# Kernel optimization log

Hardware: AMD Instinct MI355X
Metric: run time of the kernel (lower is better)

The kernel has to match this reference:

```python
import jax, jax.numpy as jnp
import numpy as np

INP_DIM = 1024
PROJ_DIM = 1024
SEQ = 2048
BATCH = 4

def setup_inputs() -> dict:
    key = jax.random.key(0)
    k1, k2, k3, k4 = jax.random.split(key, 4)
    inputs = jax.random.normal(k1, (BATCH, SEQ, INP_DIM), dtype=jnp.float32)
    # nn.Linear weights stored as (out, in); we keep them that way and transpose in matmul
    Wq = jax.random.normal(k2, (PROJ_DIM, INP_DIM), dtype=jnp.float32) * (1.0 / np.sqrt(INP_DIM))
    Wk = jax.random.normal(k3, (PROJ_DIM, INP_DIM), dtype=jnp.float32) * (1.0 / np.sqrt(INP_DIM))
    Wv = jax.random.normal(k4, (PROJ_DIM, INP_DIM), dtype=jnp.float32) * (1.0 / np.sqrt(INP_DIM))
    return {"inputs": inputs, "Wq": Wq, "Wk": Wk, "Wv": Wv}

def reference(inputs, Wq, Wk, Wv):
    # QKV projections: x @ W.T (nn.Linear convention)
    Q = jnp.einsum('bsd,pd->bsp', inputs, Wq)
    K = jnp.einsum('bsd,pd->bsp', inputs, Wk)
    V = jnp.einsum('bsd,pd->bsp', inputs, Wv)
    scores = jnp.einsum('bqp,bkp->bqk', Q, K)  # [B, S, S]
    n = inputs.shape[1]
    causal = jnp.tril(jnp.ones((n, n), dtype=bool))  # True = keep
    scores = jnp.where(causal, scores, -jnp.inf)
    weights = jax.nn.softmax(scores / jnp.sqrt(jnp.float32(Q.shape[-1])), axis=-1)
    # dropout rate = 0.0 -> identity
    Z = jnp.einsum('bqk,bkp->bqp', weights, V)
    return Z
```

## Files before the change

kernel.cpp:

```cpp
#include <hip/hip_runtime.h>
#include <stdint.h>

#define SEQ   2048
#define DIM   1024
#define BATCH 4

typedef _Float16 f16;
typedef __attribute__((ext_vector_type(8))) _Float16 f16x8;
typedef __attribute__((ext_vector_type(4))) _Float16 f16x4;
typedef __attribute__((ext_vector_type(4))) float   f32x4;

typedef void __attribute__((address_space(1))) vg_t;
typedef void __attribute__((address_space(3))) vl_t;

__device__ __forceinline__ void gld16(const void* g, void* l) {
  __builtin_amdgcn_global_load_lds((vg_t*)g, (vl_t*)l, 16, 0, 0);
}

__global__ __launch_bounds__(256) void cvt_all(const float* __restrict__ x,
                                               const float* __restrict__ wq,
                                               const float* __restrict__ wk,
                                               const float* __restrict__ wv,
                                               f16* __restrict__ xb,
                                               f16* __restrict__ wh) {
  const int bx = blockIdx.x;
  const float* in; f16* out; int base;
  if (bx < 8192)       { in = x;  out = xb;             base = bx; }
  else if (bx < 9216)  { in = wq; out = wh;             base = bx - 8192; }
  else if (bx < 10240) { in = wk; out = wh + (1 << 20); base = bx - 9216; }
  else                 { in = wv; out = wh + (2 << 20); base = bx - 10240; }
  const long i = ((long)base * 256 + threadIdx.x) * 4;
  float4 v = *(const float4*)(in + i);
  f16x4 o = { (f16)v.x, (f16)v.y, (f16)v.z, (f16)v.w };
  *(f16x4*)(out + i) = o;
}

template <int MODE, int CAUSAL, int BK>
__global__ __launch_bounds__(256) void gemm_bt(const f16* __restrict__ A, int lda, long aOffZ,
                                               const f16* __restrict__ B, int ldb, long bOffZ,
                                               void* __restrict__ Cv, int ldc, long cOffZ,
                                               int K) {
  constexpr int CH  = BK / 8;
  constexpr int RPL = 64 / CH;
  constexpr int NL  = 32 / RPL;
  __shared__ __align__(16) f16 lA[128 * BK];
  __shared__ __align__(16) f16 lB[128 * BK];

  const int tid  = threadIdx.x;
  const int wave = tid >> 6;
  const int lane = tid & 63;

  int m0, n0, z;
  if (CAUSAL == 3) {
    const int id   = blockIdx.x;
    const int item = (id < 256) ? id : 767 - id;
    const int mt   = 15 - (item >> 5);
    const int j    = item & 31;
    m0 = mt * 128;
    n0 = (j & 7) * 128;
    z  = j >> 3;
  } else {
    m0 = blockIdx.x * 128;
    n0 = blockIdx.y * 128;
    z  = blockIdx.z;
  }

  if (CAUSAL == 1 && n0 >= m0 + 128) return;
  const int Keff = (CAUSAL >= 2) ? (m0 + 128) : K;

  const f16* Ab = A + (long)z * aOffZ + (long)m0 * lda;
  const f16* Bb = B + (long)z * bOffZ + (long)n0 * ldb;

  const int wm = (wave & 1) * 64;
  const int wn = (wave >> 1) * 64;

  f32x4 acc[4][4] = {};

  const int srow = lane / CH;
  const int sj   = lane % CH;
  const int fr   = lane & 15;
  const int fq   = lane >> 4;

  for (int kt = 0; kt < Keff; kt += BK) {
    __syncthreads();
#pragma unroll
    for (int j = 0; j < NL; ++j) {
      const int rgrp = j * 4 + wave;
      const int row  = rgrp * RPL + srow;
      const int gch  = sj ^ (row & (CH - 1));
      gld16(Ab + (long)row * lda + kt + gch * 8, (void*)(lA + rgrp * 512 + lane * 8));
      gld16(Bb + (long)row * ldb + kt + gch * 8, (void*)(lB + rgrp * 512 + lane * 8));
    }
    __syncthreads();

#pragma unroll
    for (int kk = 0; kk < BK; kk += 32) {
      f16x8 af[4], bf[4];
#pragma unroll
      for (int i = 0; i < 4; ++i) {
        const int arow = wm + i * 16 + fr;
        const int ach  = (kk / 8 + fq) ^ (arow & (CH - 1));
        af[i] = *(const f16x8*)(lA + arow * BK + ach * 8);
        const int brow = wn + i * 16 + fr;
        const int bch  = (kk / 8 + fq) ^ (brow & (CH - 1));
        bf[i] = *(const f16x8*)(lB + brow * BK + bch * 8);
      }
#pragma unroll
      for (int mi = 0; mi < 4; ++mi)
#pragma unroll
        for (int ni = 0; ni < 4; ++ni)
          acc[mi][ni] = __builtin_amdgcn_mfma_f32_16x16x32_f16(af[mi], bf[ni], acc[mi][ni], 0, 0, 0);
    }
  }

#pragma unroll
  for (int mi = 0; mi < 4; ++mi) {
    const int row = m0 + wm + mi * 16 + fq * 4;
#pragma unroll
    for (int ni = 0; ni < 4; ++ni) {
      const int col = n0 + wn + ni * 16 + fr;
      if constexpr (MODE == 0) {
        float* C = (float*)Cv + (long)z * cOffZ;
#pragma unroll
        for (int r = 0; r < 4; ++r) C[(long)(row + r) * ldc + col] = acc[mi][ni][r];
      } else if constexpr (MODE == 1) {
        f16* C = (f16*)Cv + (long)z * cOffZ;
#pragma unroll
        for (int r = 0; r < 4; ++r) C[(long)(row + r) * ldc + col] = (f16)acc[mi][ni][r];
      } else if constexpr (MODE == 2) {
        f16* C = (f16*)Cv + (long)z * cOffZ;
        f16x4 o = { (f16)acc[mi][ni][0], (f16)acc[mi][ni][1],
                    (f16)acc[mi][ni][2], (f16)acc[mi][ni][3] };
        *(f16x4*)(C + (long)col * ldc + row) = o;
      } else {
        f16* Qh  = (f16*)Cv;
        f16* Kh  = Qh + (size_t)8 * 1024 * 1024;
        f16* VTb = Kh + (size_t)8 * 1024 * 1024;
        if (col < 1024) {
#pragma unroll
          for (int r = 0; r < 4; ++r) Qh[(long)(row + r) * DIM + col] = (f16)acc[mi][ni][r];
        } else if (col < 2048) {
#pragma unroll
          for (int r = 0; r < 4; ++r) Kh[(long)(row + r) * DIM + (col - 1024)] = (f16)acc[mi][ni][r];
        } else {
          f16x4 o = { (f16)acc[mi][ni][0], (f16)acc[mi][ni][1],
                      (f16)acc[mi][ni][2], (f16)acc[mi][ni][3] };
          *(f16x4*)(VTb + (long)(col - 2048) * (BATCH * SEQ) + row) = o;
        }
      }
    }
  }
}

__global__ __launch_bounds__(256) void softmax_causal(f16* S) {
  const int q = blockIdx.x, b = blockIdx.y;
  f16* row = S + ((long)b * SEQ + q) * SEQ;
  const int tid = threadIdx.x;
  const int lane = tid & 63, wave = tid >> 6;
  const int nvalid = q + 1;

  f16x8 vv = {};
  if (tid * 8 < nvalid) vv = *(const f16x8*)(row + tid * 8);
  float v[8];
  float m = -3.0e38f;
#pragma unroll
  for (int i = 0; i < 8; ++i) {
    const int k = tid * 8 + i;
    v[i] = (k < nvalid) ? (float)vv[i] * 0.03125f : -3.0e38f;
    m = fmaxf(m, v[i]);
  }
#pragma unroll
  for (int off = 32; off; off >>= 1) m = fmaxf(m, __shfl_xor(m, off));
  __shared__ float redm[4], reds[4];
  if (lane == 0) redm[wave] = m;
  __syncthreads();
  m = fmaxf(fmaxf(redm[0], redm[1]), fmaxf(redm[2], redm[3]));

  float s = 0.f;
#pragma unroll
  for (int i = 0; i < 8; ++i) {
    const float p = (v[i] > -1.0e37f) ? __expf(v[i] - m) : 0.f;
    v[i] = p;
    s += p;
  }
#pragma unroll
  for (int off = 32; off; off >>= 1) s += __shfl_xor(s, off);
  if (lane == 0) reds[wave] = s;
  __syncthreads();
  s = reds[0] + reds[1] + reds[2] + reds[3];
  const float inv = 1.f / s;
  f16x8 o;
#pragma unroll
  for (int i = 0; i < 8; ++i) o[i] = (f16)(v[i] * inv);
  *(f16x8*)(row + tid * 8) = o;
}

extern "C" void kernel_launch(void* const* d_in, const int* in_sizes, int n_in,
                              void* d_out, int out_size, void* d_ws, size_t ws_size,
                              hipStream_t stream) {
  const float* x  = (const float*)d_in[0];
  const float* Wq = (const float*)d_in[1];
  const float* Wk = (const float*)d_in[2];
  const float* Wv = (const float*)d_in[3];
  float* out = (float*)d_out;

  if (ws_size < (size_t)51 * 1024 * 1024 * 2) return;

  f16* xb = (f16*)d_ws;
  f16* Wh = xb + (size_t)8 * 1024 * 1024;
  f16* Qh = Wh + (size_t)3 * 1024 * 1024;
  f16* Kh = Qh + (size_t)8 * 1024 * 1024;
  f16* VT = Kh + (size_t)8 * 1024 * 1024;
  f16* Sc = VT + (size_t)8 * 1024 * 1024;

  const long QOFF = (long)SEQ * DIM;
  const long SOFF = (long)SEQ * SEQ;

  cvt_all<<<11264, 256, 0, stream>>>(x, Wq, Wk, Wv, xb, Wh);

  gemm_bt<3, 0, 64><<<dim3(64, 24, 1), 256, 0, stream>>>(xb, DIM, 0, Wh, DIM, 0, Qh, 0, 0, DIM);

  gemm_bt<1, 1, 64><<<dim3(16, 16, 4), 256, 0, stream>>>(Qh, DIM, QOFF, Kh, DIM, QOFF,
                                                         Sc, SEQ, SOFF, DIM);

  softmax_causal<<<dim3(SEQ, BATCH), 256, 0, stream>>>(Sc);

  gemm_bt<0, 3, 64><<<dim3(512, 1, 1), 256, 0, stream>>>(Sc, SEQ, SOFF,
                                                         VT, BATCH * SEQ, SEQ,
                                                         out, DIM, (long)SEQ * DIM, SEQ);
}
```

Before: 255.1 us.

## Add 256x256 eight-wave pipelined QKV GEMM and widen BK for attention GEMMs

```diff
diff --git a/kernel.cpp b/kernel.cpp
--- a/kernel.cpp
+++ b/kernel.cpp
@@ -35,6 +35,145 @@
   *(f16x4*)(out + i) = o;
 }
 
+__global__ __launch_bounds__(512, 2) void qkv_8ph(const f16* __restrict__ A,
+                                                  const f16* __restrict__ B,
+                                                  f16* __restrict__ Qh) {
+  __shared__ __align__(16) f16 ls[4][16384];
+
+  const int tid  = threadIdx.x;
+  const int wave = tid >> 6;
+  const int lane = tid & 63;
+  const int fr   = lane & 15;
+  const int fq   = lane >> 4;
+
+  const int lin = blockIdx.x;
+  const int swz = (lin & 7) * 48 + (lin >> 3);
+  const int m0  = (swz / 12) * 256;
+  const int n0  = (swz % 12) * 256;
+
+  const f16* Ab = A + (long)m0 * DIM;
+  const f16* Bb = B + (long)n0 * DIM;
+
+  const int wm = (wave & 1) * 128;
+  const int wn = (wave >> 1) * 64;
+
+  f16* lA0 = &ls[0][0]; f16* lB0 = &ls[1][0];
+  f16* lA1 = &ls[2][0]; f16* lB1 = &ls[3][0];
+
+  f32x4 acc[8][4] = {};
+  f16x8 af[4][2], b0[2][2], b1[2][2];
+
+#define STAGE(gb, lb, t, h)                                                    \
+  {                                                                            \
+    const int rr_ = tid >> 3, sj_ = tid & 7;                                   \
+    _Pragma("unroll") for (int i_ = 0; i_ < 2; ++i_) {                         \
+      const int row_ = (h) * 128 + i_ * 64 + rr_;                              \
+      gld16(gb + (long)row_ * DIM + (t) * 64 + ((sj_ ^ (row_ & 7)) << 3),      \
+            (void*)((lb) + (h) * 8192 + i_ * 4096 + tid * 8));                 \
+    }                                                                          \
+  }
+
+#define LDA(lsrc, q)                                                           \
+  {                                                                            \
+    _Pragma("unroll") for (int mi_ = 0; mi_ < 4; ++mi_) {                      \
+      const int row_ = wm + (q) * 64 + mi_ * 16 + fr;                          \
+      _Pragma("unroll") for (int x_ = 0; x_ < 2; ++x_)                         \
+        af[mi_][x_] = *(const f16x8*)((lsrc) + row_ * 64 +                     \
+                                      (((x_ * 4 + fq) ^ (row_ & 7)) << 3));    \
+    }                                                                          \
+  }
+
+#define LDB(lsrc, breg, s)                                                     \
+  {                                                                            \
+    _Pragma("unroll") for (int nj_ = 0; nj_ < 2; ++nj_) {                      \
+      const int row_ = wn + (s) * 32 + nj_ * 16 + fr;                          \
+      _Pragma("unroll") for (int x_ = 0; x_ < 2; ++x_)                         \
+        breg[nj_][x_] = *(const f16x8*)((lsrc) + row_ * 64 +                   \
+                                        (((x_ * 4 + fq) ^ (row_ & 7)) << 3));  \
+    }                                                                          \
+  }
+
+#define MM(q, s, breg)                                                         \
+  {                                                                            \
+    __builtin_amdgcn_s_setprio(1);                                             \
+    _Pragma("unroll") for (int mi_ = 0; mi_ < 4; ++mi_)                        \
+    _Pragma("unroll") for (int nj_ = 0; nj_ < 2; ++nj_)                        \
+    _Pragma("unroll") for (int x_ = 0; x_ < 2; ++x_)                           \
+      acc[(q) * 4 + mi_][(s) * 2 + nj_] = __builtin_amdgcn_mfma_f32_16x16x32_f16( \
+          af[mi_][x_], breg[nj_][x_], acc[(q) * 4 + mi_][(s) * 2 + nj_], 0, 0, 0); \
+    __builtin_amdgcn_s_setprio(0);                                             \
+  }
+
+#define BAR() __builtin_amdgcn_s_barrier()
+#define VMW(n) asm volatile("s_waitcnt vmcnt(" #n ")" ::: "memory")
+
+  STAGE(Bb, lB0, 0, 0); STAGE(Ab, lA0, 0, 0);
+  STAGE(Bb, lB0, 0, 1); STAGE(Ab, lA0, 0, 1);
+  STAGE(Bb, lB1, 1, 0); STAGE(Bb, lB1, 1, 1);
+  VMW(4);
+  BAR();
+
+  for (int j = 0; j < 8; ++j) {
+    const int t0 = 2 * j;
+    const bool nl = (j < 7);
+
+    LDA(lA0, 0); LDB(lB0, b0, 0);
+    STAGE(Ab, lA1, t0 + 1, 0);
+    BAR(); MM(0, 0, b0); BAR();
+    LDB(lB0, b1, 1);
+    STAGE(Ab, lA1, t0 + 1, 1);
+    BAR(); MM(0, 1, b1); BAR();
+    LDA(lA0, 1);
+    if (nl) STAGE(Bb, lB0, t0 + 2, 0);
+    BAR(); MM(1, 1, b1); BAR();
+    if (nl) STAGE(Ab, lA0, t0 + 2, 0);
+    BAR(); MM(1, 0, b0);
+    if (nl) { VMW(4); } else { VMW(0); }
+    BAR();
+    LDA(lA1, 0); LDB(lB1, b0, 0);
+    if (nl) STAGE(Bb, lB0, t0 + 2, 1);
+    BAR(); MM(0, 0, b0); BAR();
+    LDB(lB1, b1, 1);
+    if (nl) STAGE(Ab, lA0, t0 + 2, 1);
+    BAR(); MM(0, 1, b1); BAR();
+    LDA(lA1, 1);
+    if (nl) STAGE(Bb, lB1, t0 + 3, 0);
+    BAR(); MM(1, 1, b1); BAR();
+    if (nl) STAGE(Bb, lB1, t0 + 3, 1);
+    BAR(); MM(1, 0, b0);
+    if (nl) { VMW(4); BAR(); }
+  }
+
+#undef STAGE
+#undef LDA
+#undef LDB
+#undef MM
+#undef BAR
+#undef VMW
+
+  f16* Kh = Qh + (size_t)8 * 1024 * 1024;
+  f16* VT = Kh + (size_t)8 * 1024 * 1024;
+#pragma unroll
+  for (int mi = 0; mi < 8; ++mi) {
+    const int row = m0 + wm + mi * 16 + fq * 4;
+#pragma unroll
+    for (int ni = 0; ni < 4; ++ni) {
+      const int col = n0 + wn + ni * 16 + fr;
+      if (n0 < 1024) {
+#pragma unroll
+        for (int r = 0; r < 4; ++r) Qh[(long)(row + r) * DIM + col] = (f16)acc[mi][ni][r];
+      } else if (n0 < 2048) {
+#pragma unroll
+        for (int r = 0; r < 4; ++r) Kh[(long)(row + r) * DIM + (col - 1024)] = (f16)acc[mi][ni][r];
+      } else {
+        f16x4 o = { (f16)acc[mi][ni][0], (f16)acc[mi][ni][1],
+                    (f16)acc[mi][ni][2], (f16)acc[mi][ni][3] };
+        *(f16x4*)(VT + (long)(col - 2048) * (BATCH * SEQ) + row) = o;
+      }
+    }
+  }
+}
+
 template <int MODE, int CAUSAL, int BK>
 __global__ __launch_bounds__(256) void gemm_bt(const f16* __restrict__ A, int lda, long aOffZ,
                                                const f16* __restrict__ B, int ldb, long bOffZ,
@@ -127,26 +266,11 @@
         f16* C = (f16*)Cv + (long)z * cOffZ;
 #pragma unroll
         for (int r = 0; r < 4; ++r) C[(long)(row + r) * ldc + col] = (f16)acc[mi][ni][r];
-      } else if constexpr (MODE == 2) {
+      } else {
         f16* C = (f16*)Cv + (long)z * cOffZ;
         f16x4 o = { (f16)acc[mi][ni][0], (f16)acc[mi][ni][1],
                     (f16)acc[mi][ni][2], (f16)acc[mi][ni][3] };
         *(f16x4*)(C + (long)col * ldc + row) = o;
-      } else {
-        f16* Qh  = (f16*)Cv;
-        f16* Kh  = Qh + (size_t)8 * 1024 * 1024;
-        f16* VTb = Kh + (size_t)8 * 1024 * 1024;
-        if (col < 1024) {
-#pragma unroll
-          for (int r = 0; r < 4; ++r) Qh[(long)(row + r) * DIM + col] = (f16)acc[mi][ni][r];
-        } else if (col < 2048) {
-#pragma unroll
-          for (int r = 0; r < 4; ++r) Kh[(long)(row + r) * DIM + (col - 1024)] = (f16)acc[mi][ni][r];
-        } else {
-          f16x4 o = { (f16)acc[mi][ni][0], (f16)acc[mi][ni][1],
-                      (f16)acc[mi][ni][2], (f16)acc[mi][ni][3] };
-          *(f16x4*)(VTb + (long)(col - 2048) * (BATCH * SEQ) + row) = o;
-        }
       }
     }
   }
@@ -218,14 +342,14 @@
 
   cvt_all<<<11264, 256, 0, stream>>>(x, Wq, Wk, Wv, xb, Wh);
 
-  gemm_bt<3, 0, 64><<<dim3(64, 24, 1), 256, 0, stream>>>(xb, DIM, 0, Wh, DIM, 0, Qh, 0, 0, DIM);
-
-  gemm_bt<1, 1, 64><<<dim3(16, 16, 4), 256, 0, stream>>>(Qh, DIM, QOFF, Kh, DIM, QOFF,
-                                                         Sc, SEQ, SOFF, DIM);
+  qkv_8ph<<<384, 512, 0, stream>>>(xb, Wh, Qh);
+
+  gemm_bt<1, 1, 128><<<dim3(16, 16, 4), 256, 0, stream>>>(Qh, DIM, QOFF, Kh, DIM, QOFF,
+                                                          Sc, SEQ, SOFF, DIM);
 
   softmax_causal<<<dim3(SEQ, BATCH), 256, 0, stream>>>(Sc);
 
-  gemm_bt<0, 3, 64><<<dim3(512, 1, 1), 256, 0, stream>>>(Sc, SEQ, SOFF,
-                                                         VT, BATCH * SEQ, SEQ,
-                                                         out, DIM, (long)SEQ * DIM, SEQ);
-}
+  gemm_bt<0, 3, 128><<<dim3(512, 1, 1), 256, 0, stream>>>(Sc, SEQ, SOFF,
+                                                          VT, BATCH * SEQ, SEQ,
+                                                          out, DIM, (long)SEQ * DIM, SEQ);
+}
```

New measurement: 237.4 us. 7.0% less time.

## Add triple-buffered 128x256 QKV projection kernel and raise BK for attention GEMMs

Applied to the files above, without the earlier changes.

```diff
diff --git a/kernel.cpp b/kernel.cpp
--- a/kernel.cpp
+++ b/kernel.cpp
@@ -35,6 +35,125 @@
   *(f16x4*)(out + i) = o;
 }
 
+__global__ __launch_bounds__(512, 2) void qkv_p3(const f16* __restrict__ A,
+                                                 const f16* __restrict__ B,
+                                                 f16* __restrict__ Qh) {
+  __shared__ __align__(16) f16 ls[3][24576];
+
+  const int tid  = threadIdx.x;
+  const int wave = tid >> 6;
+  const int lane = tid & 63;
+  const int fr   = lane & 15;
+  const int fq   = lane >> 4;
+
+  const int lin = blockIdx.x;
+  const int swz = (lin & 7) * 96 + (lin >> 3);
+  const int m0  = (swz / 12) * 128;
+  const int n0  = (swz % 12) * 256;
+
+  const f16* Ab = A + (long)m0 * DIM;
+  const f16* Bb = B + (long)n0 * DIM;
+
+  const int wm = (wave & 1) * 64;
+  const int wn = (wave >> 1) * 64;
+
+  f32x4 acc[4][4] = {};
+  f16x8 af[4], bf[4];
+
+#define STAGE(t, c)                                                            \
+  {                                                                            \
+    const int rr_ = tid >> 3, sj_ = tid & 7;                                   \
+    f16* lb_ = &ls[(t) % 3][0];                                                \
+    if ((c) < 2) {                                                             \
+      const int row_ = (c) * 64 + rr_;                                         \
+      gld16(Ab + (long)row_ * DIM + (t) * 64 + ((sj_ ^ (row_ & 7)) << 3),      \
+            (void*)(lb_ + (c) * 4096 + tid * 8));                              \
+    } else {                                                                   \
+      const int row_ = ((c) - 2) * 64 + rr_;                                   \
+      gld16(Bb + (long)row_ * DIM + (t) * 64 + ((sj_ ^ (row_ & 7)) << 3),      \
+            (void*)(lb_ + 8192 + ((c) - 2) * 4096 + tid * 8));                 \
+    }                                                                          \
+  }
+
+#define LDF(p, ks)                                                             \
+  {                                                                            \
+    const f16* lAx_ = &ls[p][0];                                               \
+    const f16* lBx_ = &ls[p][8192];                                            \
+    _Pragma("unroll") for (int mi_ = 0; mi_ < 4; ++mi_) {                      \
+      const int r_ = wm + mi_ * 16 + fr;                                       \
+      af[mi_] = *(const f16x8*)(lAx_ + r_ * 64 +                               \
+                                ((((ks) * 4 + fq) ^ (r_ & 7)) << 3));          \
+    }                                                                          \
+    _Pragma("unroll") for (int ni_ = 0; ni_ < 4; ++ni_) {                      \
+      const int r_ = wn + ni_ * 16 + fr;                                       \
+      bf[ni_] = *(const f16x8*)(lBx_ + r_ * 64 +                               \
+                                ((((ks) * 4 + fq) ^ (r_ & 7)) << 3));          \
+    }                                                                          \
+  }
+
+#define MMAC()                                                                 \
+  {                                                                            \
+    __builtin_amdgcn_s_setprio(1);                                             \
+    _Pragma("unroll") for (int mi_ = 0; mi_ < 4; ++mi_)                        \
+    _Pragma("unroll") for (int ni_ = 0; ni_ < 4; ++ni_)                        \
+      acc[mi_][ni_] = __builtin_amdgcn_mfma_f32_16x16x32_f16(                  \
+          af[mi_], bf[ni_], acc[mi_][ni_], 0, 0, 0);                           \
+    __builtin_amdgcn_s_setprio(0);                                             \
+  }
+
+#define BAR() __builtin_amdgcn_s_barrier()
+#define VMW(n) asm volatile("s_waitcnt vmcnt(" #n ")" ::: "memory")
+
+#pragma unroll
+  for (int c = 0; c < 6; ++c) STAGE(0, c);
+#pragma unroll
+  for (int c = 0; c < 6; ++c) STAGE(1, c);
+  VMW(6);
+  BAR();
+
+#pragma unroll
+  for (int t = 0; t < 14; ++t) {
+    LDF(t % 3, 0);
+    STAGE(t + 2, 0); STAGE(t + 2, 1); STAGE(t + 2, 2);
+    BAR(); MMAC(); BAR();
+    LDF(t % 3, 1);
+    STAGE(t + 2, 3); STAGE(t + 2, 4); STAGE(t + 2, 5);
+    BAR(); MMAC(); VMW(6); BAR();
+  }
+  LDF(2, 0); BAR(); MMAC(); BAR();
+  LDF(2, 1); BAR(); MMAC(); VMW(0); BAR();
+  LDF(0, 0); BAR(); MMAC(); BAR();
+  LDF(0, 1); BAR(); MMAC();
+
+#undef STAGE
+#undef LDF
+#undef MMAC
+#undef BAR
+#undef VMW
+
+  f16* Kh = Qh + (size_t)8 * 1024 * 1024;
+  f16* VT = Kh + (size_t)8 * 1024 * 1024;
+#pragma unroll
+  for (int mi = 0; mi < 4; ++mi) {
+    const int row = m0 + wm + mi * 16 + fq * 4;
+#pragma unroll
+    for (int ni = 0; ni < 4; ++ni) {
+      const int col = n0 + wn + ni * 16 + fr;
+      if (n0 < 1024) {
+#pragma unroll
+        for (int r = 0; r < 4; ++r) Qh[(long)(row + r) * DIM + col] = (f16)acc[mi][ni][r];
+      } else if (n0 < 2048) {
+#pragma unroll
+        for (int r = 0; r < 4; ++r) Kh[(long)(row + r) * DIM + (col - 1024)] = (f16)acc[mi][ni][r];
+      } else {
+        f16x4 o = { (f16)acc[mi][ni][0], (f16)acc[mi][ni][1],
+                    (f16)acc[mi][ni][2], (f16)acc[mi][ni][3] };
+        *(f16x4*)(VT + (long)(col - 2048) * (BATCH * SEQ) + row) = o;
+      }
+    }
+  }
+}
+
 template <int MODE, int CAUSAL, int BK>
 __global__ __launch_bounds__(256) void gemm_bt(const f16* __restrict__ A, int lda, long aOffZ,
                                                const f16* __restrict__ B, int ldb, long bOffZ,
@@ -127,26 +246,11 @@
         f16* C = (f16*)Cv + (long)z * cOffZ;
 #pragma unroll
         for (int r = 0; r < 4; ++r) C[(long)(row + r) * ldc + col] = (f16)acc[mi][ni][r];
-      } else if constexpr (MODE == 2) {
+      } else {
         f16* C = (f16*)Cv + (long)z * cOffZ;
         f16x4 o = { (f16)acc[mi][ni][0], (f16)acc[mi][ni][1],
                     (f16)acc[mi][ni][2], (f16)acc[mi][ni][3] };
         *(f16x4*)(C + (long)col * ldc + row) = o;
-      } else {
-        f16* Qh  = (f16*)Cv;
-        f16* Kh  = Qh + (size_t)8 * 1024 * 1024;
-        f16* VTb = Kh + (size_t)8 * 1024 * 1024;
-        if (col < 1024) {
-#pragma unroll
-          for (int r = 0; r < 4; ++r) Qh[(long)(row + r) * DIM + col] = (f16)acc[mi][ni][r];
-        } else if (col < 2048) {
-#pragma unroll
-          for (int r = 0; r < 4; ++r) Kh[(long)(row + r) * DIM + (col - 1024)] = (f16)acc[mi][ni][r];
-        } else {
-          f16x4 o = { (f16)acc[mi][ni][0], (f16)acc[mi][ni][1],
-                      (f16)acc[mi][ni][2], (f16)acc[mi][ni][3] };
-          *(f16x4*)(VTb + (long)(col - 2048) * (BATCH * SEQ) + row) = o;
-        }
       }
     }
   }
@@ -218,14 +322,14 @@
 
   cvt_all<<<11264, 256, 0, stream>>>(x, Wq, Wk, Wv, xb, Wh);
 
-  gemm_bt<3, 0, 64><<<dim3(64, 24, 1), 256, 0, stream>>>(xb, DIM, 0, Wh, DIM, 0, Qh, 0, 0, DIM);
-
-  gemm_bt<1, 1, 64><<<dim3(16, 16, 4), 256, 0, stream>>>(Qh, DIM, QOFF, Kh, DIM, QOFF,
-                                                         Sc, SEQ, SOFF, DIM);
+  qkv_p3<<<768, 512, 0, stream>>>(xb, Wh, Qh);
+
+  gemm_bt<1, 1, 128><<<dim3(16, 16, 4), 256, 0, stream>>>(Qh, DIM, QOFF, Kh, DIM, QOFF,
+                                                          Sc, SEQ, SOFF, DIM);
 
   softmax_causal<<<dim3(SEQ, BATCH), 256, 0, stream>>>(Sc);
 
-  gemm_bt<0, 3, 64><<<dim3(512, 1, 1), 256, 0, stream>>>(Sc, SEQ, SOFF,
-                                                         VT, BATCH * SEQ, SEQ,
-                                                         out, DIM, (long)SEQ * DIM, SEQ);
-}
+  gemm_bt<0, 3, 128><<<dim3(512, 1, 1), 256, 0, stream>>>(Sc, SEQ, SOFF,
+                                                          VT, BATCH * SEQ, SEQ,
+                                                          out, DIM, (long)SEQ * DIM, SEQ);
+}
```

Result: faster. 241.5 us (-5.3%).

## Add pipelined 256x192 QKV GEMM kernel, widen BK to 128, trim softmax stores

Applied to the files above, without the earlier changes.

```diff
diff --git a/kernel.cpp b/kernel.cpp
--- a/kernel.cpp
+++ b/kernel.cpp
@@ -35,6 +35,132 @@
   *(f16x4*)(out + i) = o;
 }
 
+__global__ __launch_bounds__(512, 2) void qkv_192(const f16* __restrict__ A,
+                                                  const f16* __restrict__ B,
+                                                  f16* __restrict__ Qh) {
+  __shared__ __align__(16) f16 sA[2][16384];
+  __shared__ __align__(16) f16 sB[3][12288];
+
+  const int tid  = threadIdx.x;
+  const int wave = tid >> 6;
+  const int lane = tid & 63;
+  const int fr   = lane & 15;
+  const int fq   = lane >> 4;
+  const int rr   = tid >> 3;
+  const int sj   = tid & 7;
+
+  const int id  = blockIdx.x;
+  const int swz = (id & 7) * 64 + (id >> 3);
+  const int m0  = (swz >> 4) * 256;
+  const int n0  = (swz & 15) * 192;
+
+  const f16* Ab = A + (long)m0 * DIM;
+  const f16* Bb = B + (long)n0 * DIM;
+
+  const int wm = (wave & 1) * 128;
+  const int wn = (wave >> 1) * 48;
+
+  f32x4 acc[8][3] = {};
+  f16x8 af[8], bf[3];
+
+#define STAGE_A(t)                                                             \
+  {                                                                            \
+    _Pragma("unroll") for (int u_ = 0; u_ < 4; ++u_) {                         \
+      const int row_ = u_ * 64 + rr;                                           \
+      gld16(Ab + (long)row_ * DIM + (t) * 64 + ((sj ^ (row_ & 7)) << 3),       \
+            (void*)(&sA[(t) & 1][0] + u_ * 4096 + tid * 8));                   \
+    }                                                                          \
+  }
+#define STAGE_B(t)                                                             \
+  {                                                                            \
+    _Pragma("unroll") for (int u_ = 0; u_ < 3; ++u_) {                         \
+      const int row_ = u_ * 64 + rr;                                           \
+      gld16(Bb + (long)row_ * DIM + (t) * 64 + ((sj ^ (row_ & 7)) << 3),       \
+            (void*)(&sB[(t) % 3][0] + u_ * 4096 + tid * 8));                   \
+    }                                                                          \
+  }
+#define LDFA(pa, ks)                                                           \
+  {                                                                            \
+    _Pragma("unroll") for (int mi_ = 0; mi_ < 8; ++mi_) {                      \
+      const int r_ = wm + mi_ * 16 + fr;                                       \
+      af[mi_] = *(const f16x8*)(&sA[pa][0] + r_ * 64 +                         \
+                                ((((ks) * 4 + fq) ^ (r_ & 7)) << 3));          \
+    }                                                                          \
+  }
+#define LDFB(pb, ks)                                                           \
+  {                                                                            \
+    _Pragma("unroll") for (int ni_ = 0; ni_ < 3; ++ni_) {                      \
+      const int r_ = wn + ni_ * 16 + fr;                                       \
+      bf[ni_] = *(const f16x8*)(&sB[pb][0] + r_ * 64 +                         \
+                                ((((ks) * 4 + fq) ^ (r_ & 7)) << 3));          \
+    }                                                                          \
+  }
+#define MM()                                                                   \
+  {                                                                            \
+    __builtin_amdgcn_s_setprio(1);                                             \
+    _Pragma("unroll") for (int mi_ = 0; mi_ < 8; ++mi_)                        \
+    _Pragma("unroll") for (int ni_ = 0; ni_ < 3; ++ni_)                        \
+      acc[mi_][ni_] = __builtin_amdgcn_mfma_f32_16x16x32_f16(                  \
+          af[mi_], bf[ni_], acc[mi_][ni_], 0, 0, 0);                           \
+    __builtin_amdgcn_s_setprio(0);                                             \
+  }
+#define BAR() __builtin_amdgcn_s_barrier()
+#define VMW(n) asm volatile("s_waitcnt vmcnt(" #n ")" ::: "memory")
+
+  STAGE_A(0); STAGE_B(0); STAGE_B(1);
+  VMW(3);
+  BAR();
+
+#pragma unroll
+  for (int t = 0; t < 14; ++t) {
+    LDFA(t & 1, 0); LDFB(t % 3, 0);
+    STAGE_A(t + 1);
+    BAR(); MM(); BAR();
+    LDFA(t & 1, 1); LDFB(t % 3, 1);
+    STAGE_B(t + 2);
+    BAR(); MM(); VMW(3); BAR();
+  }
+  LDFA(0, 0); LDFB(2, 0);
+  STAGE_A(15);
+  BAR(); MM(); BAR();
+  LDFA(0, 1); LDFB(2, 1);
+  BAR(); MM(); VMW(0); BAR();
+  LDFA(1, 0); LDFB(0, 0);
+  BAR(); MM(); BAR();
+  LDFA(1, 1); LDFB(0, 1);
+  BAR(); MM();
+
+#undef STAGE_A
+#undef STAGE_B
+#undef LDFA
+#undef LDFB
+#undef MM
+#undef BAR
+#undef VMW
+
+  f16* Kh = Qh + (size_t)8 * 1024 * 1024;
+  f16* VT = Kh + (size_t)8 * 1024 * 1024;
+#pragma unroll
+  for (int mi = 0; mi < 8; ++mi) {
+    const int row = m0 + wm + mi * 16 + fq * 4;
+#pragma unroll
+    for (int ni = 0; ni < 3; ++ni) {
+      const int col = n0 + wn + ni * 16 + fr;
+      if (col < 1024) {
+#pragma unroll
+        for (int r = 0; r < 4; ++r) Qh[(long)(row + r) * DIM + col] = (f16)acc[mi][ni][r];
+      } else if (col < 2048) {
+#pragma unroll
+        for (int r = 0; r < 4; ++r) Kh[(long)(row + r) * DIM + (col - 1024)] = (f16)acc[mi][ni][r];
+      } else {
+        f16x4 o = { (f16)acc[mi][ni][0], (f16)acc[mi][ni][1],
+                    (f16)acc[mi][ni][2], (f16)acc[mi][ni][3] };
+        *(f16x4*)(VT + (long)(col - 2048) * (BATCH * SEQ) + row) = o;
+      }
+    }
+  }
+}
+
 template <int MODE, int CAUSAL, int BK>
 __global__ __launch_bounds__(256) void gemm_bt(const f16* __restrict__ A, int lda, long aOffZ,
                                                const f16* __restrict__ B, int ldb, long bOffZ,
@@ -127,26 +253,11 @@
         f16* C = (f16*)Cv + (long)z * cOffZ;
 #pragma unroll
         for (int r = 0; r < 4; ++r) C[(long)(row + r) * ldc + col] = (f16)acc[mi][ni][r];
-      } else if constexpr (MODE == 2) {
+      } else {
         f16* C = (f16*)Cv + (long)z * cOffZ;
         f16x4 o = { (f16)acc[mi][ni][0], (f16)acc[mi][ni][1],
                     (f16)acc[mi][ni][2], (f16)acc[mi][ni][3] };
         *(f16x4*)(C + (long)col * ldc + row) = o;
-      } else {
-        f16* Qh  = (f16*)Cv;
-        f16* Kh  = Qh + (size_t)8 * 1024 * 1024;
-        f16* VTb = Kh + (size_t)8 * 1024 * 1024;
-        if (col < 1024) {
-#pragma unroll
-          for (int r = 0; r < 4; ++r) Qh[(long)(row + r) * DIM + col] = (f16)acc[mi][ni][r];
-        } else if (col < 2048) {
-#pragma unroll
-          for (int r = 0; r < 4; ++r) Kh[(long)(row + r) * DIM + (col - 1024)] = (f16)acc[mi][ni][r];
-        } else {
-          f16x4 o = { (f16)acc[mi][ni][0], (f16)acc[mi][ni][1],
-                      (f16)acc[mi][ni][2], (f16)acc[mi][ni][3] };
-          *(f16x4*)(VTb + (long)(col - 2048) * (BATCH * SEQ) + row) = o;
-        }
       }
     }
   }
@@ -158,6 +269,7 @@
   const int tid = threadIdx.x;
   const int lane = tid & 63, wave = tid >> 6;
   const int nvalid = q + 1;
+  const int kneed  = ((q >> 7) + 1) << 7;
 
   f16x8 vv = {};
   if (tid * 8 < nvalid) vv = *(const f16x8*)(row + tid * 8);
@@ -192,7 +304,7 @@
   f16x8 o;
 #pragma unroll
   for (int i = 0; i < 8; ++i) o[i] = (f16)(v[i] * inv);
-  *(f16x8*)(row + tid * 8) = o;
+  if (tid * 8 < kneed) *(f16x8*)(row + tid * 8) = o;
 }
 
 extern "C" void kernel_launch(void* const* d_in, const int* in_sizes, int n_in,
@@ -218,14 +330,14 @@
 
   cvt_all<<<11264, 256, 0, stream>>>(x, Wq, Wk, Wv, xb, Wh);
 
-  gemm_bt<3, 0, 64><<<dim3(64, 24, 1), 256, 0, stream>>>(xb, DIM, 0, Wh, DIM, 0, Qh, 0, 0, DIM);
-
-  gemm_bt<1, 1, 64><<<dim3(16, 16, 4), 256, 0, stream>>>(Qh, DIM, QOFF, Kh, DIM, QOFF,
-                                                         Sc, SEQ, SOFF, DIM);
+  qkv_192<<<512, 512, 0, stream>>>(xb, Wh, Qh);
+
+  gemm_bt<1, 1, 128><<<dim3(16, 16, 4), 256, 0, stream>>>(Qh, DIM, QOFF, Kh, DIM, QOFF,
+                                                          Sc, SEQ, SOFF, DIM);
 
   softmax_causal<<<dim3(SEQ, BATCH), 256, 0, stream>>>(Sc);
 
-  gemm_bt<0, 3, 64><<<dim3(512, 1, 1), 256, 0, stream>>>(Sc, SEQ, SOFF,
-                                                         VT, BATCH * SEQ, SEQ,
-                                                         out, DIM, (long)SEQ * DIM, SEQ);
-}
+  gemm_bt<0, 3, 128><<<dim3(512, 1, 1), 256, 0, stream>>>(Sc, SEQ, SOFF,
+                                                          VT, BATCH * SEQ, SEQ,
+                                                          out, DIM, (long)SEQ * DIM, SEQ);
+}
```

Measured after the change: 238.6 us. 1.07x faster.
